# Optimization experiments

Hardware: AMD Instinct MI355X
Metric: run time of the kernel (lower is better)

## Reference

```python
import jax, jax.numpy as jnp
import numpy as np

B, S, D = 8, 1024, 768
H = 12
DH = D // H  # 64
SCALE = 1.0 / (D ** 0.5)  # module scales by full embedding_dim, not head_dim


def setup_inputs() -> dict:
    key = jax.random.key(0)
    ks = jax.random.split(key, 7)
    std = 1.0 / np.sqrt(D)
    return {
        "x": jax.random.normal(ks[0], (B, S, D), dtype=jnp.float32),
        "Wq": jax.random.uniform(ks[1], (D, D), jnp.float32, -std, std),
        "bq": jax.random.uniform(ks[2], (D,), jnp.float32, -std, std),
        "Wk": jax.random.uniform(ks[3], (D, D), jnp.float32, -std, std),
        "bk": jax.random.uniform(ks[4], (D,), jnp.float32, -std, std),
        "Wv": jax.random.uniform(ks[5], (D, D), jnp.float32, -std, std),
        "bv": jax.random.uniform(ks[6], (D,), jnp.float32, -std, std),
    }


def reference(x, Wq, bq, Wk, bk, Wv, bv):
    b, s, d = x.shape
    # projections; torch.chunk(dim=-1) == reshape last dim to [H, DH]
    q = (x @ Wq + bq).reshape(b, s, H, DH)
    k = (x @ Wk + bk).reshape(b, s, H, DH)
    v = (x @ Wv + bv).reshape(b, s, H, DH)
    # per-head scores [b, h, s, s], scaled by sqrt(embedding_dim) per source
    scores = jnp.einsum("bqhd,bkhd->bhqk", q, k) * SCALE
    attn = jax.nn.softmax(scores, axis=-1)
    out = jnp.einsum("bhqk,bkhd->bqhd", attn, v)
    # concat heads back along last dim (order matches chunk order)
    return out.reshape(b, s, d)
```

## Files before the change

### kernel.cpp

```cpp
#include <hip/hip_runtime.h>
#include <cstdint>
#include <cstddef>

typedef unsigned short u16;
typedef unsigned int u32;
typedef unsigned char u8;

using bfx8 = __attribute__((ext_vector_type(8))) __bf16;
using floatx16 = __attribute__((ext_vector_type(16))) float;

static constexpr int kS = 1024;
static constexpr int kD = 768;
static constexpr int kH = 12;
static constexpr int kDH = 64;
#define SCALE 0.036084391824351614f

__device__ __forceinline__ u16 f2bf(float f) {
    u32 u = __float_as_uint(f);
    return (u16)((u + 0x7fffu + ((u >> 16) & 1u)) >> 16);
}

__device__ __forceinline__ void gld16(const void* g, void* l) {
    __builtin_amdgcn_global_load_lds(
        (__attribute__((address_space(1))) const u32*)g,
        (__attribute__((address_space(3))) u32*)l, 16, 0, 0);
}

__global__ __launch_bounds__(256) void cvt(const float* __restrict__ x, u16* __restrict__ xb,
                                           const float* __restrict__ w0, const float* __restrict__ w1,
                                           const float* __restrict__ w2, u16* __restrict__ wt) {
    __shared__ float t[32][33];
    int bid = blockIdx.x;
    if (bid < 6144) {
        int i = (bid * 256 + threadIdx.x) * 4;
        float4 v = *(const float4*)(x + i);
        u32 lo = (u32)f2bf(v.x) | ((u32)f2bf(v.y) << 16);
        u32 hi = (u32)f2bf(v.z) | ((u32)f2bf(v.w) << 16);
        *(uint2*)(xb + i) = make_uint2(lo, hi);
    } else {
        int idx = bid - 6144;
        int z = idx / 576;
        int rem = idx - z * 576;
        int by = rem / 24, bx = rem - by * 24;
        const float* W = z == 0 ? w0 : (z == 1 ? w1 : w2);
        u16* dst = wt + (size_t)z * kD * kD;
        int k0 = bx * 32, n0 = by * 32;
        int tx = threadIdx.x & 31, ty = threadIdx.x >> 5;
#pragma unroll
        for (int j = 0; j < 4; j++)
            t[ty + j * 8][tx] = W[(size_t)(k0 + ty + j * 8) * kD + n0 + tx];
        __syncthreads();
#pragma unroll
        for (int j = 0; j < 4; j++)
            dst[(size_t)(n0 + ty + j * 8) * kD + k0 + tx] = f2bf(t[tx][ty + j * 8]);
    }
}

__global__ __launch_bounds__(256) void proj(const u16* __restrict__ xb, const u16* __restrict__ wt,
                                            const float* __restrict__ bq, const float* __restrict__ bk,
                                            const float* __restrict__ bvp,
                                            u16* __restrict__ qb, u16* __restrict__ kb, u16* __restrict__ vt) {
    __shared__ u16 As0[128 * 64];
    __shared__ u16 Bs0[128 * 64];
    __shared__ u16 As1[128 * 64];
    __shared__ u16 Bs1[128 * 64];
    int orig = blockIdx.x;
    int wg = (orig & 7) * 144 + (orig >> 3);
    int mt = wg / 18, nt = wg - mt * 18;
    int m0 = mt * 128;
    int n0g = nt * 128;
    int t = threadIdx.x;
    int w = t >> 6, lane = t & 63;
    int l31 = lane & 31, hi = lane >> 5;
    int wm = (w & 1) * 64, wn = (w >> 1) * 64;
    int rloc8 = lane >> 3, p8 = lane & 7;
    int chw = p8 ^ rloc8;
    const u16* Brow = wt + (size_t)n0g * kD;
    int swz = l31 & 7;
    floatx16 acc[2][2] = {};

    auto STAGE = [&](u16* Ad, u16* Bd, int ks) {
#pragma unroll
        for (int i = 0; i < 4; i++) {
            int j = w * 4 + i;
            int r = 8 * j + rloc8;
            gld16(xb + (size_t)(m0 + r) * kD + ks + chw * 8, Ad + j * 512);
            gld16(Brow + (size_t)r * kD + ks + chw * 8, Bd + j * 512);
        }
    };
    auto COMP = [&](const u16* Ad, const u16* Bd) {
#pragma unroll
        for (int s = 0; s < 4; s++) {
            int tc = ((s * 2 + hi) ^ swz) * 8;
            bfx8 a[2], bf[2];
#pragma unroll
            for (int i = 0; i < 2; i++) {
                a[i] = *(const bfx8*)&Ad[(wm + i * 32 + l31) * 64 + tc];
                bf[i] = *(const bfx8*)&Bd[(wn + i * 32 + l31) * 64 + tc];
            }
#pragma unroll
            for (int i = 0; i < 2; i++)
#pragma unroll
                for (int j2 = 0; j2 < 2; j2++)
                    acc[i][j2] = __builtin_amdgcn_mfma_f32_32x32x16_bf16(a[i], bf[j2], acc[i][j2], 0, 0, 0);
        }
    };

    STAGE(As0, Bs0, 0);
    __syncthreads();
    for (int kk = 0; kk < 5; kk++) {
        STAGE(As1, Bs1, 64 + 128 * kk);
        COMP(As0, Bs0);
        __syncthreads();
        STAGE(As0, Bs0, 128 + 128 * kk);
        COMP(As1, Bs1);
        __syncthreads();
    }
    STAGE(As1, Bs1, 704);
    COMP(As0, Bs0);
    __syncthreads();
    COMP(As1, Bs1);

    int zz = nt / 6;
    int nl0 = (nt - zz * 6) * 128;
    const float* bias = zz == 0 ? bq : (zz == 1 ? bk : bvp);
    float mul = zz == 0 ? SCALE : 1.0f;
#pragma unroll
    for (int j = 0; j < 2; j++) {
        int nl = nl0 + wn + j * 32 + l31;
        float bb = bias[nl];
#pragma unroll
        for (int i = 0; i < 2; i++) {
            int mbase = m0 + wm + i * 32 + 4 * hi;
            if (zz < 2) {
                u16* dst = zz == 0 ? qb : kb;
#pragma unroll
                for (int reg = 0; reg < 16; reg++) {
                    int m = mbase + (reg & 3) + 8 * (reg >> 2);
                    dst[(size_t)m * kD + nl] = f2bf((acc[i][j][reg] + bb) * mul);
                }
            } else {
                int hh = nl >> 6, dh = nl & 63;
#pragma unroll
                for (int g = 0; g < 4; g++) {
                    int m = (m0 + wm + i * 32) + 4 * (g & 1) + 8 * hi + 16 * (g >> 1);
                    int bi = m >> 10, s = m & 1023;
                    u32 lo = (u32)f2bf(acc[i][j][4 * g + 0] + bb) | ((u32)f2bf(acc[i][j][4 * g + 1] + bb) << 16);
                    u32 h2 = (u32)f2bf(acc[i][j][4 * g + 2] + bb) | ((u32)f2bf(acc[i][j][4 * g + 3] + bb) << 16);
                    *(uint2*)&vt[(((size_t)bi * kH + hh) * kDH + dh) * kS + s] = make_uint2(lo, h2);
                }
            }
        }
    }
}

__global__ __launch_bounds__(256, 3) void attn(const u16* __restrict__ qb, const u16* __restrict__ kb,
                                               const u16* __restrict__ vt, float* __restrict__ out) {
    __shared__ u16 Ks[2][64 * 64];
    __shared__ u16 Vs[2][64 * 64];
    __shared__ float Lw[128];
    int orig = blockIdx.x;
    int wg = (orig & 7) * 96 + (orig >> 3);
    int bh = wg >> 3;
    int q0 = (wg & 7) * 128;
    int b = bh / kH, h = bh % kH;
    int t = threadIdx.x, w = t >> 6, lane = t & 63;
    int l31 = lane & 31, hi = lane >> 5;
    int swz = l31 & 7;

    bfx8 qf[4];
    {
        const u16* qrow = qb + (size_t)(b * kS + q0 + w * 32 + l31) * kD + h * kDH + hi * 8;
#pragma unroll
        for (int f = 0; f < 4; f++) qf[f] = *(const bfx8*)(qrow + f * 16);
    }

    auto STAGE = [&](int db, int kt) {
        int kk0 = kt * 64;
#pragma unroll
        for (int i = 0; i < 2; i++) {
            int jj = 2 * w + i;
            int r = 8 * jj + (lane >> 3);
            int c = (lane & 7) ^ ((lane >> 3) & 7);
            gld16(kb + (size_t)(b * kS + kk0 + r) * kD + h * kDH + c * 8, &Ks[db][jj * 512]);
        }
#pragma unroll
        for (int i = 0; i < 2; i++) {
            int jj = 2 * w + i;
            int r = 8 * jj + (lane >> 3);
            int c = (lane & 7) ^ ((lane >> 3) & 7);
            gld16(vt + (((size_t)b * kH + h) * kDH + r) * kS + kk0 + c * 8, &Vs[db][jj * 512]);
        }
    };

    float rsum = 0.f;
    floatx16 oacc[2] = {};

    STAGE(0, 0);
    __syncthreads();

    int cur = 0;
    for (int kt = 0; kt < 16; kt++) {
        if (kt < 15) STAGE(cur ^ 1, kt + 1);

        const u16* Kc = Ks[cur];
        const u8* Vc = (const u8*)Vs[cur];

        floatx16 sacc[2] = {};
        __builtin_amdgcn_s_setprio(1);
#pragma unroll
        for (int s2 = 0; s2 < 4; s2++) {
#pragma unroll
            for (int fm = 0; fm < 2; fm++) {
                bfx8 ak = *(const bfx8*)&Kc[(fm * 32 + l31) * 64 + ((s2 * 2 + hi) ^ swz) * 8];
                sacc[fm] = __builtin_amdgcn_mfma_f32_32x32x16_bf16(ak, qf[s2], sacc[fm], 0, 0, 0);
            }
        }
        __builtin_amdgcn_s_setprio(0);

        bfx8 pa[2][2];
#pragma unroll
        for (int fm = 0; fm < 2; fm++) {
#pragma unroll
            for (int hh = 0; hh < 2; hh++) {
                bfx8 pv;
#pragma unroll
                for (int jj = 0; jj < 8; jj++) {
                    float e = __expf(sacc[fm][8 * hh + jj]);
                    rsum += e;
                    pv[jj] = (__bf16)e;
                }
                pa[fm][hh] = pv;
            }
        }

        __builtin_amdgcn_s_setprio(1);
#pragma unroll
        for (int s = 0; s < 4; s++) {
#pragma unroll
            for (int db = 0; db < 2; db++) {
                bfx8 bv = *(const bfx8*)(Vc + (db * 32 + l31) * 128 + (((s * 2 + hi) ^ swz) * 16));
                oacc[db] = __builtin_amdgcn_mfma_f32_32x32x16_bf16(pa[s >> 1][s & 1], bv, oacc[db], 0, 0, 0);
            }
        }
        __builtin_amdgcn_s_setprio(0);

        __syncthreads();
        cur ^= 1;
    }

    rsum += __shfl_xor(rsum, 32, 64);
    if (lane < 32) Lw[w * 32 + lane] = rsum;
    __syncthreads();
#pragma unroll
    for (int g = 0; g < 4; g++) {
#pragma unroll
        for (int r2 = 0; r2 < 4; r2++) {
            int qloc = w * 32 + 4 * hi + r2 + 8 * g;
            float linv = 1.0f / Lw[qloc];
#pragma unroll
            for (int db = 0; db < 2; db++) {
                out[(size_t)(b * kS + q0 + qloc) * kD + h * kDH + db * 32 + l31] = oacc[db][4 * g + r2] * linv;
            }
        }
    }
}

extern "C" void kernel_launch(void* const* d_in, const int* in_sizes, int n_in,
                              void* d_out, int out_size, void* d_ws, size_t ws_size,
                              hipStream_t stream) {
    const float* x  = (const float*)d_in[0];
    const float* Wq = (const float*)d_in[1];
    const float* bq = (const float*)d_in[2];
    const float* Wk = (const float*)d_in[3];
    const float* bk = (const float*)d_in[4];
    const float* Wv = (const float*)d_in[5];
    const float* bv = (const float*)d_in[6];
    float* out = (float*)d_out;

    u16* ws = (u16*)d_ws;
    u16* xb = ws;
    u16* wt = xb + 6291456;
    u16* qb = wt + 1769472;
    u16* kb = qb + 6291456;
    u16* vt = kb + 6291456;

    cvt<<<dim3(7872), dim3(256), 0, stream>>>(x, xb, Wq, Wk, Wv, wt);
    proj<<<dim3(1152), dim3(256), 0, stream>>>(xb, wt, bq, bk, bv, qb, kb, vt);
    attn<<<dim3(768), dim3(256), 0, stream>>>(qb, kb, vt, out);
}
```

Measured before the change: 166.4 us.

## Triple-buffer K/V tiles with vmcnt waits and fold log2e into Q scale

Result: slower. 174.8 us (+5.0%).

```diff
diff --git a/kernel.cpp b/kernel.cpp
--- a/kernel.cpp
+++ b/kernel.cpp
@@ -13,7 +13,7 @@
 static constexpr int kD = 768;
 static constexpr int kH = 12;
 static constexpr int kDH = 64;
-#define SCALE 0.036084391824351614f
+#define QSCALE 0.05205877458947922f
 
 __device__ __forceinline__ u16 f2bf(float f) {
     u32 u = __float_as_uint(f);
@@ -25,6 +25,8 @@
         (__attribute__((address_space(1))) const u32*)g,
         (__attribute__((address_space(3))) u32*)l, 16, 0, 0);
 }
+
+#define VMW(n) asm volatile("s_waitcnt vmcnt(" #n ")" ::: "memory")
 
 __global__ __launch_bounds__(256) void cvt(const float* __restrict__ x, u16* __restrict__ xb,
                                            const float* __restrict__ w0, const float* __restrict__ w1,
@@ -124,7 +126,7 @@
     int zz = nt / 6;
     int nl0 = (nt - zz * 6) * 128;
     const float* bias = zz == 0 ? bq : (zz == 1 ? bk : bvp);
-    float mul = zz == 0 ? SCALE : 1.0f;
+    float mul = zz == 0 ? QSCALE : 1.0f;
 #pragma unroll
     for (int j = 0; j < 2; j++) {
         int nl = nl0 + wn + j * 32 + l31;
@@ -156,8 +158,8 @@
 
 __global__ __launch_bounds__(256, 3) void attn(const u16* __restrict__ qb, const u16* __restrict__ kb,
                                                const u16* __restrict__ vt, float* __restrict__ out) {
-    __shared__ u16 Ks[2][64 * 64];
-    __shared__ u16 Vs[2][64 * 64];
+    __shared__ u16 Ks[3 * 64 * 64];
+    __shared__ u16 Vs[3 * 64 * 64];
     __shared__ float Lw[128];
     int orig = blockIdx.x;
     int wg = (orig & 7) * 96 + (orig >> 3);
@@ -177,19 +179,15 @@
 
     auto STAGE = [&](int db, int kt) {
         int kk0 = kt * 64;
+        u16* Kd = Ks + db * 4096;
+        u16* Vd = Vs + db * 4096;
 #pragma unroll
         for (int i = 0; i < 2; i++) {
             int jj = 2 * w + i;
             int r = 8 * jj + (lane >> 3);
             int c = (lane & 7) ^ ((lane >> 3) & 7);
-            gld16(kb + (size_t)(b * kS + kk0 + r) * kD + h * kDH + c * 8, &Ks[db][jj * 512]);
-        }
-#pragma unroll
-        for (int i = 0; i < 2; i++) {
-            int jj = 2 * w + i;
-            int r = 8 * jj + (lane >> 3);
-            int c = (lane & 7) ^ ((lane >> 3) & 7);
-            gld16(vt + (((size_t)b * kH + h) * kDH + r) * kS + kk0 + c * 8, &Vs[db][jj * 512]);
+            gld16(kb + (size_t)(b * kS + kk0 + r) * kD + h * kDH + c * 8, Kd + jj * 512);
+            gld16(vt + (((size_t)b * kH + h) * kDH + r) * kS + kk0 + c * 8, Vd + jj * 512);
         }
     };
 
@@ -197,14 +195,17 @@
     floatx16 oacc[2] = {};
 
     STAGE(0, 0);
-    __syncthreads();
-
-    int cur = 0;
+    STAGE(1, 1);
+    VMW(4);
+    __builtin_amdgcn_s_barrier();
+    __builtin_amdgcn_sched_barrier(0);
+
+    int cur = 0, sb = 2;
     for (int kt = 0; kt < 16; kt++) {
-        if (kt < 15) STAGE(cur ^ 1, kt + 1);
-
-        const u16* Kc = Ks[cur];
-        const u8* Vc = (const u8*)Vs[cur];
+        if (kt < 14) STAGE(sb, kt + 2);
+
+        const u16* Kc = Ks + cur * 4096;
+        const u8* Vc = (const u8*)(Vs + cur * 4096);
 
         floatx16 sacc[2] = {};
         __builtin_amdgcn_s_setprio(1);
@@ -226,7 +227,7 @@
                 bfx8 pv;
 #pragma unroll
                 for (int jj = 0; jj < 8; jj++) {
-                    float e = __expf(sacc[fm][8 * hh + jj]);
+                    float e = __builtin_exp2f(sacc[fm][8 * hh + jj]);
                     rsum += e;
                     pv[jj] = (__bf16)e;
                 }
@@ -245,8 +246,13 @@
         }
         __builtin_amdgcn_s_setprio(0);
 
-        __syncthreads();
-        cur ^= 1;
+        if (kt < 14) { VMW(4); } else { VMW(0); }
+        if (kt < 15) {
+            __builtin_amdgcn_s_barrier();
+            __builtin_amdgcn_sched_barrier(0);
+        }
+        cur = (cur == 2) ? 0 : cur + 1;
+        sb = (sb == 2) ? 0 : sb + 1;
     }
 
     rsum += __shfl_xor(rsum, 32, 64);
```
